# Kernel tuning notes

Hardware: AMD Instinct MI355X
Metric: run time of the kernel (lower is better)

## Reference

```python
import jax, jax.numpy as jnp
import numpy as np
import math


def _lsq(x, s, bit, all_positive):
    # LSQ fake-quant: scale -> clamp -> round (STE) -> dequant
    if all_positive:
        qn, qp = 0.0, float(2 ** bit - 1)
    else:
        qn, qp = -float(2 ** (bit - 1)), float(2 ** (bit - 1) - 1)
    g = 1.0 / math.sqrt(x.size * qp)  # grad-scale factor (static)
    sg = s * g
    s_eff = sg + jax.lax.stop_gradient(s - sg)  # fwd = s, grad scaled by g
    xq = jnp.clip(x / s_eff, qn, qp)
    xq = xq + jax.lax.stop_gradient(jnp.round(xq) - xq)  # round with STE
    return xq * s_eff


def _conv(x, w, stride):
    return jax.lax.conv_general_dilated(
        x, w, window_strides=(stride, stride), padding='VALID',
        dimension_numbers=('NCHW', 'OIHW', 'NCHW'))


def setup_inputs() -> dict:
    key = jax.random.key(0)
    ks = jax.random.split(key, 5)
    B = 65536
    x = jax.random.normal(ks[0], (B, 1, 28, 28), dtype=jnp.float32)
    w1 = jax.random.normal(ks[1], (4, 1, 5, 5), dtype=jnp.float32) * 0.2
    w2 = jax.random.normal(ks[2], (8, 4, 3, 3), dtype=jnp.float32) * 0.2
    fc_w = jax.random.normal(ks[3], (10, 200), dtype=jnp.float32) * 0.07
    fc_b = jax.random.normal(ks[4], (10,), dtype=jnp.float32) * 0.01
    one = jnp.ones((1,), dtype=jnp.float32)
    return {"x": x, "w1": w1, "w2": w2, "fc_w": fc_w, "fc_b": fc_b,
            "s_in": one * 0.05, "s_w1": one * 0.02, "s_a1": one * 0.05,
            "s_w2": one * 0.02, "s_a2": one * 0.05, "s_fc": one * 0.02}


def reference(x, w1, w2, fc_w, fc_b, s_in, s_w1, s_a1, s_w2, s_a2, s_fc):
    x = _lsq(x, s_in, 8, False)
    x = _conv(x, _lsq(w1, s_w1, 8, False), 2)          # [B,4,12,12]
    x = jax.nn.relu(_lsq(x, s_a1, 8, True))
    x = _conv(x, _lsq(w2, s_w2, 8, False), 2)          # [B,8,5,5]
    x = jax.nn.relu(_lsq(x, s_a2, 8, True))
    x = x.reshape(x.shape[0], -1)                      # [B,200]
    return x @ _lsq(fc_w, s_fc, 8, False).T + fc_b     # [B,10]
```

## Files before the change

### kernel.cpp

```cpp
#include <hip/hip_runtime.h>
#include <math.h>

#define G  8
#define NG 4

#if __has_builtin(__builtin_amdgcn_sdot4)
__device__ __forceinline__ int dot4(unsigned a, unsigned b, int c) {
    return __builtin_amdgcn_sdot4((int)a, (int)b, c, false);
}
#else
__device__ __forceinline__ int dot4(unsigned a, unsigned b, int c) {
    c += (int)(signed char)(a & 255u)         * (int)(signed char)(b & 255u);
    c += (int)(signed char)((a >> 8) & 255u)  * (int)(signed char)((b >> 8) & 255u);
    c += (int)(signed char)((a >> 16) & 255u) * (int)(signed char)((b >> 16) & 255u);
    c += (int)(signed char)(a >> 24)          * (int)(signed char)(b >> 24);
    return c;
}
#endif

__device__ __forceinline__ float seff(float s, float gf) {
    float sg = s * gf;
    return sg + (s - sg);
}
__device__ __forceinline__ unsigned q8(float v, float s, float rs) {
    float q0 = v * rs;
    float r  = fmaf(-s, q0, v);
    float y  = fmaf(r, rs, q0);
    y = fminf(fmaxf(y, -128.f), 127.f);
    float t = y + 12582912.0f;
    return __float_as_uint(t);
}
__device__ __forceinline__ int mround(int acc, double r) {
    double t = fma((double)acc, r, 6755399441055744.0);
    return (int)__double_as_longlong(t);
}

extern "C" __global__ __launch_bounds__(256, 4)
void qcnn_fused(const float* __restrict__ x,  const float* __restrict__ w1,
                const float* __restrict__ w2, const float* __restrict__ fcw,
                const float* __restrict__ fcb,
                const float* __restrict__ s_in, const float* __restrict__ s_w1,
                const float* __restrict__ s_a1, const float* __restrict__ s_w2,
                const float* __restrict__ s_a2, const float* __restrict__ s_fc,
                float* __restrict__ out, int B,
                float gx, float gw1, float ga1, float gw2, float ga2, float gfc)
{
    __shared__ unsigned xs[2][G*196];
    __shared__ unsigned a1p[G*144];
    __shared__ unsigned a2p[G*50];
    __shared__ unsigned w1pk[4][5][4];
    __shared__ unsigned w2p[8][9];
    __shared__ unsigned fcp[10][50];
    __shared__ int K2s[8];
    __shared__ int K3s[10];
    __shared__ float fcbs[10];

    const int tid = threadIdx.x;
    const int g   = tid >> 5;
    const int t   = tid & 31;

    const float sx  = seff(s_in[0], gx);
    const float sw1 = seff(s_w1[0], gw1);
    const float sa1 = seff(s_a1[0], ga1);
    const float sw2 = seff(s_w2[0], gw2);
    const float sa2 = seff(s_a2[0], ga2);
    const float sfc = seff(s_fc[0], gfc);
    const float rsx = 1.0f / sx;
    const float rw1 = 1.0f / sw1;
    const float rw2 = 1.0f / sw2;
    const float rfc = 1.0f / sfc;
    const double r1 = (double)sx  * (double)sw1 / (double)sa1;
    const double r2 = (double)sa1 * (double)sw2 / (double)sa2;
    const double r3 = (double)sa2 * (double)sfc;

    if (tid < 80) {
        const int c = tid / 20, rem = tid % 20, ky = rem >> 2, vv = rem & 3;
        const float* wr = w1 + c*25 + ky*5;
        unsigned b[5];
        #pragma unroll
        for (int k = 0; k < 5; ++k) b[k] = q8(wr[k], sw1, rw1) & 255u;
        unsigned pk;
        if      (vv == 0) pk = b[0] | (b[1] << 8) | (b[2] << 16) | (b[3] << 24);
        else if (vv == 1) pk = b[4];
        else if (vv == 2) pk = (b[0] << 16) | (b[1] << 24);
        else              pk = b[2] | (b[3] << 8) | (b[4] << 16);
        w1pk[c][ky][vv] = pk;
    } else if (tid < 152) {
        const int d = tid - 80, oc = d / 9, tap = d % 9;
        unsigned pk = 0;
        #pragma unroll
        for (int ic = 0; ic < 4; ++ic)
            pk |= (q8(w2[oc*36 + ic*9 + tap], sw2, rw2) & 255u) << (8*ic);
        w2p[oc][tap] = pk;
    }
    if (tid < 10) fcbs[tid] = fcb[tid];
    for (int i = tid; i < 500; i += 256) {
        const int o = i / 50, kd = i % 50;
        const float* fr = fcw + o*200 + kd*4;
        unsigned pk = 0;
        #pragma unroll
        for (int k = 0; k < 4; ++k)
            pk |= (q8(fr[k], sfc, rfc) & 255u) << (8*k);
        fcp[o][kd] = pk;
    }
    __syncthreads();
    if (tid < 8) {
        int s = 0;
        #pragma unroll
        for (int d = 0; d < 9; ++d) s = dot4(w2p[tid][d], 0x01010101u, s);
        K2s[tid] = s << 7;
    } else if (tid < 18) {
        const int o = tid - 8;
        int s = 0;
        for (int d = 0; d < 50; ++d) s = dot4(fcp[o][d], 0x01010101u, s);
        K3s[o] = s << 7;
    }

    const long long gbase = (long long)blockIdx.x * NG;

    auto stage = [&](long long grp, int buf) {
        const int nimg = (B - (int)(grp * G) < G) ? (B - (int)(grp * G)) : G;
        if (nimg <= 0) return;
        const float4* xg = (const float4*)x + grp * (G * 196 / G) * G / 4 * 0
                           ;
        (void)xg;
        const float4* xp = (const float4*)x + grp * (long long)(G * 196);
        unsigned* dst = xs[buf];
        if (nimg == G) {
            float4 v[6];
            #pragma unroll
            for (int k = 0; k < 6; ++k) v[k] = xp[tid + 256*k];
            const bool extra = tid < (G*196 - 6*256);
            float4 v6;
            if (extra) v6 = xp[tid + 6*256];
            #pragma unroll
            for (int k = 0; k < 6; ++k) {
                float4 w = v[k];
                dst[tid + 256*k] =
                    (q8(w.x, sx, rsx) & 255u)         |
                    ((q8(w.y, sx, rsx) & 255u) << 8)  |
                    ((q8(w.z, sx, rsx) & 255u) << 16) |
                    (q8(w.w, sx, rsx) << 24);
            }
            if (extra) {
                dst[tid + 6*256] =
                    (q8(v6.x, sx, rsx) & 255u)         |
                    ((q8(v6.y, sx, rsx) & 255u) << 8)  |
                    ((q8(v6.z, sx, rsx) & 255u) << 16) |
                    (q8(v6.w, sx, rsx) << 24);
            }
        } else {
            const int nv = nimg * 196;
            for (int i = tid; i < nv; i += 256) {
                float4 w = xp[i];
                dst[i] = (q8(w.x, sx, rsx) & 255u)         |
                         ((q8(w.y, sx, rsx) & 255u) << 8)  |
                         ((q8(w.z, sx, rsx) & 255u) << 16) |
                         (q8(w.w, sx, rsx) << 24);
            }
        }
    };

    int cur = 0;
    stage(gbase, 0);

    for (int it = 0; it < NG; ++it) {
        const long long grp = gbase + it;
        if (grp * G >= B) break;
        const int nimg = (B - (int)(grp * G) < G) ? (B - (int)(grp * G)) : G;
        __syncthreads();

        if (it + 1 < NG) stage(grp + 1, cur ^ 1);

        if (g < nimg) {
            const unsigned* xb = &xs[cur][g*196];
            #pragma unroll
            for (int k = 0; k < 3; ++k) {
                const int tau = t + 32*k;
                const int y = tau >> 3, c = (tau >> 1) & 3, h = tau & 1;
                int acc[6] = {0,0,0,0,0,0};
                #pragma unroll
                for (int ky = 0; ky < 5; ++ky) {
                    const unsigned* rp = xb + (2*y + ky)*7 + 3*h;
                    const unsigned L0 = rp[0], L1 = rp[1], L2 = rp[2], L3 = rp[3];
                    const unsigned EA = w1pk[c][ky][0], EB = w1pk[c][ky][1];
                    const unsigned OA = w1pk[c][ky][2], OB = w1pk[c][ky][3];
                    acc[0] = dot4(L1, EB, dot4(L0, EA, acc[0]));
                    acc[1] = dot4(L1, OB, dot4(L0, OA, acc[1]));
                    acc[2] = dot4(L2, EB, dot4(L1, EA, acc[2]));
                    acc[3] = dot4(L2, OB, dot4(L1, OA, acc[3]));
                    acc[4] = dot4(L3, EB, dot4(L2, EA, acc[4]));
                    acc[5] = dot4(L3, OB, dot4(L2, OA, acc[5]));
                }
                unsigned char* dst = (unsigned char*)a1p + (g*144 + y*12 + 6*h)*4 + c;
                #pragma unroll
                for (int m = 0; m < 6; ++m) {
                    int q = mround(acc[m], r1);
                    q = min(max(q, 0), 255);
                    dst[4*m] = (unsigned char)(q - 128);
                }
            }
        }
        __syncthreads();

        for (int tau = tid; tau < G*40; tau += 256) {
            const int img = tau / 40;
            const int rem = tau - img*40;
            const int oc  = rem / 5;
            const int y   = rem - oc*5;
            if (img >= nimg) break;
            unsigned wv[9];
            #pragma unroll
            for (int d = 0; d < 9; ++d) wv[d] = w2p[oc][d];
            const int k2 = K2s[oc];
            const unsigned* base = &a1p[img*144];
            unsigned rw[3][12];
            #pragma unroll
            for (int ky = 0; ky < 3; ++ky) {
                const uint4* rp = (const uint4*)&base[(2*y + ky)*12];
                uint4 A = rp[0], Bv = rp[1], Cv = rp[2];
                rw[ky][0]=A.x;  rw[ky][1]=A.y;  rw[ky][2]=A.z;  rw[ky][3]=A.w;
                rw[ky][4]=Bv.x; rw[ky][5]=Bv.y; rw[ky][6]=Bv.z; rw[ky][7]=Bv.w;
                rw[ky][8]=Cv.x; rw[ky][9]=Cv.y; rw[ky][10]=Cv.z; rw[ky][11]=Cv.w;
            }
            unsigned char* dst = (unsigned char*)a2p + img*200 + oc*25 + y*5;
            #pragma unroll
            for (int jx = 0; jx < 5; ++jx) {
                int acc = k2;
                #pragma unroll
                for (int ky = 0; ky < 3; ++ky)
                    #pragma unroll
                    for (int kx = 0; kx < 3; ++kx)
                        acc = dot4(rw[ky][2*jx + kx], wv[ky*3 + kx], acc);
                int q = mround(acc, r2);
                q = min(max(q, 0), 255);
                dst[jx] = (unsigned char)(q - 128);
            }
        }
        __syncthreads();

        if (g < nimg && t < 30) {
            const int part = t / 10;
            const int o    = t - part*10;
            const int k0   = part * 17;
            const int nk   = (part == 2) ? 16 : 17;
            int acc = 0;
            for (int ki = 0; ki < nk; ++ki) {
                const int k = k0 + ki;
                acc = dot4(a2p[g*50 + k], fcp[o][k], acc);
            }
            const int self0 = (g & 1) * 32 + o;
            const int s1 = __shfl(acc, self0 + 10);
            const int s2 = __shfl(acc, self0 + 20);
            if (part == 0) {
                const int total = acc + s1 + s2 + K3s[o];
                const double oo = (double)total * r3 + (double)fcbs[o];
                out[(grp*G + g)*10 + o] = (float)oo;
            }
        }
        cur ^= 1;
    }
}

extern "C" void kernel_launch(void* const* d_in, const int* in_sizes, int n_in,
                              void* d_out, int out_size, void* d_ws, size_t ws_size,
                              hipStream_t stream) {
    const float* x    = (const float*)d_in[0];
    const float* w1   = (const float*)d_in[1];
    const float* w2   = (const float*)d_in[2];
    const float* fcw  = (const float*)d_in[3];
    const float* fcb  = (const float*)d_in[4];
    const float* s_in = (const float*)d_in[5];
    const float* s_w1 = (const float*)d_in[6];
    const float* s_a1 = (const float*)d_in[7];
    const float* s_w2 = (const float*)d_in[8];
    const float* s_a2 = (const float*)d_in[9];
    const float* s_fc = (const float*)d_in[10];

    const int B = in_sizes[0] / 784;
    const float gx  = (float)(1.0 / sqrt((double)B * 784.0 * 127.0));
    const float gw1 = (float)(1.0 / sqrt(100.0 * 127.0));
    const float ga1 = (float)(1.0 / sqrt((double)B * 576.0 * 255.0));
    const float gw2 = (float)(1.0 / sqrt(288.0 * 127.0));
    const float ga2 = (float)(1.0 / sqrt((double)B * 200.0 * 255.0));
    const float gfc = (float)(1.0 / sqrt(2000.0 * 127.0));

    const int imgs_per_block = G * NG;
    const int grid = (B + imgs_per_block - 1) / imgs_per_block;
    qcnn_fused<<<grid, 256, 0, stream>>>(x, w1, w2, fcw, fcb,
                                         s_in, s_w1, s_a1, s_w2, s_a2, s_fc,
                                         (float*)d_out, B,
                                         gx, gw1, ga1, gw2, ga2, gfc);
}
```

Measured before the change: 64.05 us.

## Split input staging into register prefetch and deferred LDS write, double groups per block

Input staging is split into a global load into registers issued before conv1 and a quantize-and-store into the LDS buffer issued after conv2. This lets the global memory latency overlap with the conv compute, and it removes one barrier per iteration. Each block now processes 8 groups instead of 4, which halves the grid size and amortizes the per-block weight preprocessing. Conv1 weights are loaded once per thread into registers with a fixed channel-per-lane mapping. The cost is higher register pressure from seven float4 prefetch registers held live across the conv stages, which may reduce occupancy, and fewer blocks to balance across CUs.

```diff
diff --git a/kernel.cpp b/kernel.cpp
--- a/kernel.cpp
+++ b/kernel.cpp
@@ -2,7 +2,7 @@
 #include <math.h>
 
 #define G  8
-#define NG 4
+#define NG 8
 
 #if __has_builtin(__builtin_amdgcn_sdot4)
 __device__ __forceinline__ int dot4(unsigned a, unsigned b, int c) {
@@ -29,6 +29,9 @@
     y = fminf(fmaxf(y, -128.f), 127.f);
     float t = y + 12582912.0f;
     return __float_as_uint(t);
+}
+__device__ __forceinline__ unsigned pack4(unsigned a, unsigned b, unsigned c, unsigned d) {
+    return (a & 255u) | ((b & 255u) << 8) | ((c & 255u) << 16) | (d << 24);
 }
 __device__ __forceinline__ int mround(int acc, double r) {
     double t = fma((double)acc, r, 6755399441055744.0);
@@ -48,7 +51,7 @@
     __shared__ unsigned xs[2][G*196];
     __shared__ unsigned a1p[G*144];
     __shared__ unsigned a2p[G*50];
-    __shared__ unsigned w1pk[4][5][4];
+    __shared__ __align__(16) unsigned w1pk[4][5][4];
     __shared__ unsigned w2p[8][9];
     __shared__ unsigned fcp[10][50];
     __shared__ int K2s[8];
@@ -72,6 +75,45 @@
     const double r1 = (double)sx  * (double)sw1 / (double)sa1;
     const double r2 = (double)sa1 * (double)sw2 / (double)sa2;
     const double r3 = (double)sa2 * (double)sfc;
+
+    const long long gbase = (long long)blockIdx.x * NG;
+
+    float4 Rv0, Rv1, Rv2, Rv3, Rv4, Rv5, Rv6;
+    auto stage_load = [&](long long grp) {
+        const int nimg = (B - (int)(grp * G) < G) ? (B - (int)(grp * G)) : G;
+        if (nimg != G) return;
+        const float4* xp = (const float4*)x + grp * (long long)(G * 196);
+        Rv0 = xp[tid];          Rv1 = xp[tid + 256]; Rv2 = xp[tid + 512];
+        Rv3 = xp[tid + 768];    Rv4 = xp[tid + 1024];Rv5 = xp[tid + 1280];
+        if (tid < 32) Rv6 = xp[tid + 1536];
+    };
+    auto stage_write = [&](long long grp, int buf) {
+        const int nimg = (B - (int)(grp * G) < G) ? (B - (int)(grp * G)) : G;
+        if (nimg <= 0) return;
+        unsigned* dst = xs[buf];
+        if (nimg == G) {
+            float4 v;
+            v = Rv0; dst[tid]        = pack4(q8(v.x,sx,rsx), q8(v.y,sx,rsx), q8(v.z,sx,rsx), q8(v.w,sx,rsx));
+            v = Rv1; dst[tid + 256]  = pack4(q8(v.x,sx,rsx), q8(v.y,sx,rsx), q8(v.z,sx,rsx), q8(v.w,sx,rsx));
+            v = Rv2; dst[tid + 512]  = pack4(q8(v.x,sx,rsx), q8(v.y,sx,rsx), q8(v.z,sx,rsx), q8(v.w,sx,rsx));
+            v = Rv3; dst[tid + 768]  = pack4(q8(v.x,sx,rsx), q8(v.y,sx,rsx), q8(v.z,sx,rsx), q8(v.w,sx,rsx));
+            v = Rv4; dst[tid + 1024] = pack4(q8(v.x,sx,rsx), q8(v.y,sx,rsx), q8(v.z,sx,rsx), q8(v.w,sx,rsx));
+            v = Rv5; dst[tid + 1280] = pack4(q8(v.x,sx,rsx), q8(v.y,sx,rsx), q8(v.z,sx,rsx), q8(v.w,sx,rsx));
+            if (tid < 32) {
+                v = Rv6;
+                dst[tid + 1536] = pack4(q8(v.x,sx,rsx), q8(v.y,sx,rsx), q8(v.z,sx,rsx), q8(v.w,sx,rsx));
+            }
+        } else {
+            const float4* xp = (const float4*)x + grp * (long long)(G * 196);
+            const int nv = nimg * 196;
+            for (int i = tid; i < nv; i += 256) {
+                float4 v = xp[i];
+                dst[i] = pack4(q8(v.x,sx,rsx), q8(v.y,sx,rsx), q8(v.z,sx,rsx), q8(v.w,sx,rsx));
+            }
+        }
+    };
+
+    stage_load(gbase);
 
     if (tid < 80) {
         const int c = tid / 20, rem = tid % 20, ky = rem >> 2, vv = rem & 3;
@@ -97,10 +139,8 @@
     for (int i = tid; i < 500; i += 256) {
         const int o = i / 50, kd = i % 50;
         const float* fr = fcw + o*200 + kd*4;
-        unsigned pk = 0;
-        #pragma unroll
-        for (int k = 0; k < 4; ++k)
-            pk |= (q8(fr[k], sfc, rfc) & 255u) << (8*k);
+        unsigned pk = pack4(q8(fr[0],sfc,rfc), q8(fr[1],sfc,rfc),
+                            q8(fr[2],sfc,rfc), q8(fr[3],sfc,rfc));
         fcp[o][kd] = pk;
     }
     __syncthreads();
@@ -115,82 +155,40 @@
         for (int d = 0; d < 50; ++d) s = dot4(fcp[o][d], 0x01010101u, s);
         K3s[o] = s << 7;
     }
-
-    const long long gbase = (long long)blockIdx.x * NG;
-
-    auto stage = [&](long long grp, int buf) {
-        const int nimg = (B - (int)(grp * G) < G) ? (B - (int)(grp * G)) : G;
-        if (nimg <= 0) return;
-        const float4* xg = (const float4*)x + grp * (G * 196 / G) * G / 4 * 0
-                           ;
-        (void)xg;
-        const float4* xp = (const float4*)x + grp * (long long)(G * 196);
-        unsigned* dst = xs[buf];
-        if (nimg == G) {
-            float4 v[6];
-            #pragma unroll
-            for (int k = 0; k < 6; ++k) v[k] = xp[tid + 256*k];
-            const bool extra = tid < (G*196 - 6*256);
-            float4 v6;
-            if (extra) v6 = xp[tid + 6*256];
-            #pragma unroll
-            for (int k = 0; k < 6; ++k) {
-                float4 w = v[k];
-                dst[tid + 256*k] =
-                    (q8(w.x, sx, rsx) & 255u)         |
-                    ((q8(w.y, sx, rsx) & 255u) << 8)  |
-                    ((q8(w.z, sx, rsx) & 255u) << 16) |
-                    (q8(w.w, sx, rsx) << 24);
-            }
-            if (extra) {
-                dst[tid + 6*256] =
-                    (q8(v6.x, sx, rsx) & 255u)         |
-                    ((q8(v6.y, sx, rsx) & 255u) << 8)  |
-                    ((q8(v6.z, sx, rsx) & 255u) << 16) |
-                    (q8(v6.w, sx, rsx) << 24);
-            }
-        } else {
-            const int nv = nimg * 196;
-            for (int i = tid; i < nv; i += 256) {
-                float4 w = xp[i];
-                dst[i] = (q8(w.x, sx, rsx) & 255u)         |
-                         ((q8(w.y, sx, rsx) & 255u) << 8)  |
-                         ((q8(w.z, sx, rsx) & 255u) << 16) |
-                         (q8(w.w, sx, rsx) << 24);
-            }
-        }
-    };
+    stage_write(gbase, 0);
+    __syncthreads();
 
     int cur = 0;
-    stage(gbase, 0);
-
     for (int it = 0; it < NG; ++it) {
         const long long grp = gbase + it;
         if (grp * G >= B) break;
         const int nimg = (B - (int)(grp * G) < G) ? (B - (int)(grp * G)) : G;
-        __syncthreads();
-
-        if (it + 1 < NG) stage(grp + 1, cur ^ 1);
+
+        if (it + 1 < NG) stage_load(grp + 1);
 
         if (g < nimg) {
+            const int c  = t & 3;
+            const int h  = (t >> 2) & 1;
+            const int y0 = t >> 3;
+            uint4 W[5];
+            #pragma unroll
+            for (int ky = 0; ky < 5; ++ky)
+                W[ky] = *(const uint4*)&w1pk[c][ky][0];
             const unsigned* xb = &xs[cur][g*196];
             #pragma unroll
             for (int k = 0; k < 3; ++k) {
-                const int tau = t + 32*k;
-                const int y = tau >> 3, c = (tau >> 1) & 3, h = tau & 1;
+                const int y = y0 + 4*k;
                 int acc[6] = {0,0,0,0,0,0};
                 #pragma unroll
                 for (int ky = 0; ky < 5; ++ky) {
                     const unsigned* rp = xb + (2*y + ky)*7 + 3*h;
                     const unsigned L0 = rp[0], L1 = rp[1], L2 = rp[2], L3 = rp[3];
-                    const unsigned EA = w1pk[c][ky][0], EB = w1pk[c][ky][1];
-                    const unsigned OA = w1pk[c][ky][2], OB = w1pk[c][ky][3];
-                    acc[0] = dot4(L1, EB, dot4(L0, EA, acc[0]));
-                    acc[1] = dot4(L1, OB, dot4(L0, OA, acc[1]));
-                    acc[2] = dot4(L2, EB, dot4(L1, EA, acc[2]));
-                    acc[3] = dot4(L2, OB, dot4(L1, OA, acc[3]));
-                    acc[4] = dot4(L3, EB, dot4(L2, EA, acc[4]));
-                    acc[5] = dot4(L3, OB, dot4(L2, OA, acc[5]));
+                    acc[0] = dot4(L1, W[ky].y, dot4(L0, W[ky].x, acc[0]));
+                    acc[1] = dot4(L1, W[ky].w, dot4(L0, W[ky].z, acc[1]));
+                    acc[2] = dot4(L2, W[ky].y, dot4(L1, W[ky].x, acc[2]));
+                    acc[3] = dot4(L2, W[ky].w, dot4(L1, W[ky].z, acc[3]));
+                    acc[4] = dot4(L3, W[ky].y, dot4(L2, W[ky].x, acc[4]));
+                    acc[5] = dot4(L3, W[ky].w, dot4(L2, W[ky].z, acc[5]));
                 }
                 unsigned char* dst = (unsigned char*)a1p + (g*144 + y*12 + 6*h)*4 + c;
                 #pragma unroll
@@ -237,6 +235,8 @@
                 dst[jx] = (unsigned char)(q - 128);
             }
         }
+
+        if (it + 1 < NG) stage_write(grp + 1, cur ^ 1);
         __syncthreads();
 
         if (g < nimg && t < 30) {
```

After: 59.13 us. -7.7%, faster.
